# Kernel optimization log

Measured on AMD Instinct MI355X. Metric: run time of the kernel, lower is better.

Reference implementation:

```python
import jax, jax.numpy as jnp
import numpy as np
from jax import lax

EPS = 1e-5

def _conv(x, w, pad):
    return lax.conv_general_dilated(
        x, w, window_strides=(1, 1), padding=[(pad, pad), (pad, pad)],
        dimension_numbers=('NCHW', 'OIHW', 'NCHW'))

def _bn(x, p):
    # p: [4, C] rows = gamma, beta, running_mean, running_var (inference BN)
    g, b, m, v = p[0], p[1], p[2], p[3]
    scale = g / jnp.sqrt(v + EPS)
    return x * scale[None, :, None, None] + (b - m * scale)[None, :, None, None]

def _cbr(x, w, p, relu=True):
    y = _bn(_conv(x, w, pad=1), p)
    return jax.nn.relu(y) if relu else y

def _make_bn(key, c):
    k1, k2, k3 = jax.random.split(key, 3)
    gamma = jnp.ones((c,), jnp.float32) + 0.05 * jax.random.normal(k1, (c,))
    beta = 0.1 * jax.random.normal(k2, (c,))
    mean = 0.1 * jax.random.normal(k3, (c,))
    var = jax.random.uniform(k1, (c,), minval=0.5, maxval=1.5)
    return jnp.stack([gamma, beta, mean, var]).astype(jnp.float32)

def setup_inputs() -> dict:
    key = jax.random.key(0)
    ks = jax.random.split(key, 12)
    C, M = 256, 64  # channels, bottleneck width (hard-coded 64 in source)
    B, H, W = 8, 128, 128
    s = lambda fan: 1.0 / np.sqrt(fan)
    return {
        'x': jax.random.normal(ks[0], (B, C, H, W), jnp.float32),
        'w_res': jax.random.normal(ks[1], (C, C, 1, 1), jnp.float32) * s(C),
        'bn_res': _make_bn(ks[2], C),
        'w_vpre': jax.random.normal(ks[3], (M, C, 3, 3), jnp.float32) * s(C * 9),
        'bn_vpre': _make_bn(ks[4], M),
        'w_hpre': jax.random.normal(ks[5], (M, C, 3, 3), jnp.float32) * s(C * 9),
        'bn_hpre': _make_bn(ks[6], M),
        'w_add': jax.random.normal(ks[7], (C, M, 3, 3), jnp.float32) * s(M * 9),
        'bn_add': _make_bn(ks[8], C),
        'w_post': jax.random.normal(ks[9], (C, C, 3, 3), jnp.float32) * s(C * 9),
        'bn_post': _make_bn(ks[10], C),
    }

def reference(x, w_res, bn_res, w_vpre, bn_vpre, w_hpre, bn_hpre,
              w_add, bn_add, w_post, bn_post):
    # residual branch: 1x1 conv + BN (no relu)
    res = _bn(_conv(x, w_res, pad=0), bn_res)
    # vertical branch: conv-bn-relu then TopPool (reverse cumulative max over H)
    p1 = _cbr(x, w_vpre, bn_vpre)
    pool1 = lax.cummax(p1, axis=2, reverse=True)
    # horizontal branch: conv-bn-relu then LeftPool (reverse cumulative max over W)
    p2 = _cbr(x, w_hpre, bn_hpre)
    pool2 = lax.cummax(p2, axis=3, reverse=True)
    # merge: conv-bn (no relu), residual add, relu, post conv-bn-relu
    merged = _cbr(pool1 + pool2, w_add, bn_add, relu=False)
    out = jax.nn.relu(res + merged)
    return _cbr(out, w_post, bn_post)
```

## Files before the change

### kernel.cpp

```cpp
#include <hip/hip_runtime.h>
#include <hip/hip_bf16.h>


using bf16x8  = __attribute__((ext_vector_type(8))) __bf16;
using floatx4 = __attribute__((ext_vector_type(4))) float;

typedef __attribute__((address_space(1))) const uint32_t gas_u32;
typedef __attribute__((address_space(3))) uint32_t las_u32;

__device__ __forceinline__ float bf2f(__hip_bfloat16 h) { return __bfloat162float(h); }
__device__ __forceinline__ __hip_bfloat16 f2bf(float f) { return __float2bfloat16(f); }


__global__ __launch_bounds__(256) void k_cast_x(const float* __restrict__ x,
                                                __hip_bfloat16* __restrict__ xb) {
    __shared__ float t[64][65];
    const int n  = blockIdx.z;
    const int h  = blockIdx.y;
    const int c0 = (blockIdx.x >> 1) * 64;
    const int w0 = (blockIdx.x & 1) * 64;
    const int tid = threadIdx.x;
#pragma unroll
    for (int it = 0; it < 16; ++it) {
        int idx = it * 256 + tid;
        int c = idx >> 6, w = idx & 63;
        t[c][w] = x[(((size_t)n * 256 + c0 + c) * 128 + h) * 128 + w0 + w];
    }
    __syncthreads();
#pragma unroll
    for (int it = 0; it < 16; ++it) {
        int idx = it * 256 + tid;
        int w = idx >> 6, c = idx & 63;
        xb[(((size_t)n * 128 + h) * 128 + w0 + w) * 256 + c0 + c] = f2bf(t[c][w]);
    }
}

__global__ void k_prep_bn(const float* __restrict__ p, float* __restrict__ sc,
                          float* __restrict__ bi, int C) {
    int i = blockIdx.x * 64 + threadIdx.x;
    if (i >= C) return;
    float g = p[i], b = p[C + i], m = p[2 * C + i], v = p[3 * C + i];
    float s = g / sqrtf(v + 1e-5f);
    sc[i] = s;
    bi[i] = b - m * s;
}

__global__ void k_reorder_w3(const float* __restrict__ src, __hip_bfloat16* __restrict__ dst,
                             const float* __restrict__ scale, int Cin, int CoutTot,
                             int co_off, int total) {
    int i = blockIdx.x * 256 + threadIdx.x;
    if (i >= total) return;
    int ci  = i % Cin;
    int tap = (i / Cin) % 9;
    int co  = i / (Cin * 9);
    dst[((((size_t)tap * (Cin >> 5) + (ci >> 5)) * CoutTot) + co_off + co) * 32 + (ci & 31)] =
        f2bf(src[((size_t)co * Cin + ci) * 9 + tap] * scale[co]);
}

__global__ void k_reorder_w1(const float* __restrict__ src, __hip_bfloat16* __restrict__ dst,
                             const float* __restrict__ scale, int Cin, int total) {
    int i = blockIdx.x * 256 + threadIdx.x;
    if (i >= total) return;
    dst[i] = f2bf(src[i] * scale[i / Cin]);
}


__global__ __launch_bounds__(256) void k_pool1(__hip_bfloat16* __restrict__ b) {
    const int idx = blockIdx.x * 256 + threadIdx.x;
    const int c = idx & 63;
    const int w = (idx >> 6) & 127;
    const int n = idx >> 13;
    const size_t stride = 128 * 64;
    const size_t base = ((size_t)n * 128 * 128 + w) * 64 + c;
    float m = 0.0f;
    for (int hb = 31; hb >= 0; --hb) {
        size_t a0 = base + (size_t)(4 * hb) * stride;
        float v0 = bf2f(b[a0]);
        float v1 = bf2f(b[a0 + stride]);
        float v2 = bf2f(b[a0 + 2 * stride]);
        float v3 = bf2f(b[a0 + 3 * stride]);
        float m3 = fmaxf(m, v3);
        float m2 = fmaxf(m3, v2);
        float m1 = fmaxf(m2, v1);
        float m0 = fmaxf(m1, v0);
        b[a0 + 3 * stride] = f2bf(m3);
        b[a0 + 2 * stride] = f2bf(m2);
        b[a0 + stride]     = f2bf(m1);
        b[a0]              = f2bf(m0);
        m = m0;
    }
}

__global__ __launch_bounds__(256) void k_pool2(__hip_bfloat16* __restrict__ b,
                                               const __hip_bfloat16* __restrict__ pl) {
    const int idx = blockIdx.x * 256 + threadIdx.x;
    const int c = idx & 63;
    const int h = (idx >> 6) & 127;
    const int n = idx >> 13;
    const size_t base = (((size_t)n * 128 + h) * 128) * 64 + c;
    float m = 0.0f;
    for (int wb = 31; wb >= 0; --wb) {
        size_t a0 = base + (size_t)(4 * wb) * 64;
        float v0 = bf2f(b[a0]);
        float v1 = bf2f(b[a0 + 64]);
        float v2 = bf2f(b[a0 + 128]);
        float v3 = bf2f(b[a0 + 192]);
        float u0 = bf2f(pl[a0]);
        float u1 = bf2f(pl[a0 + 64]);
        float u2 = bf2f(pl[a0 + 128]);
        float u3 = bf2f(pl[a0 + 192]);
        float m3 = fmaxf(m, v3);
        float m2 = fmaxf(m3, v2);
        float m1 = fmaxf(m2, v1);
        float m0 = fmaxf(m1, v0);
        b[a0 + 192] = f2bf(m3 + u3);
        b[a0 + 128] = f2bf(m2 + u2);
        b[a0 + 64]  = f2bf(m1 + u1);
        b[a0]       = f2bf(m0 + u0);
        m = m0;
    }
}

__global__ __launch_bounds__(256) void conv1x1(const __hip_bfloat16* __restrict__ xin,
                                               const __hip_bfloat16* __restrict__ wgt,
                                               const float* __restrict__ bias,
                                               __hip_bfloat16* __restrict__ out) {
    __shared__ __align__(16) __hip_bfloat16 Xs[128 * 64];
    __shared__ __align__(16) __hip_bfloat16 Ws[128 * 64];
    const int tid  = threadIdx.x;
    const int lane = tid & 63;
    const int wid  = tid >> 6;
    const int wm = wid >> 1, wn = wid & 1;
    const int p0 = blockIdx.x * 128;
    const int c0 = blockIdx.y * 128;
    const int q = lane >> 4, r16 = lane & 15;

    floatx4 acc[4][4] = {};

    for (int k0 = 0; k0 < 256; k0 += 64) {
#pragma unroll
        for (int it = 0; it < 4; ++it) {
            const int pp = it * 32 + (tid >> 3);
            const int g  = tid & 7;
            uint4 val = *(const uint4*)(xin + ((size_t)(p0 + pp) * 256 + k0 + g * 8));
            *(uint4*)(&Xs[pp * 64 + (((g + pp) & 7) * 8)]) = val;
        }
#pragma unroll
        for (int it = 0; it < 4; ++it) {
            const int rr = it * 32 + (tid >> 3);
            const int g  = tid & 7;
            uint4 val = *(const uint4*)(wgt + ((size_t)(c0 + rr) * 256 + k0 + g * 8));
            *(uint4*)(&Ws[rr * 64 + (((g + rr) & 7) * 8)]) = val;
        }
        __syncthreads();
#pragma unroll
        for (int ks = 0; ks < 2; ++ks) {
            bf16x8 afr[4], bfr[4];
#pragma unroll
            for (int i = 0; i < 4; ++i) {
                const int pp = wm * 64 + i * 16 + r16;
                const int g  = ks * 4 + q;
                afr[i] = *(const bf16x8*)(&Xs[pp * 64 + (((g + pp) & 7) * 8)]);
            }
#pragma unroll
            for (int j = 0; j < 4; ++j) {
                const int rr = wn * 64 + j * 16 + r16;
                const int g  = ks * 4 + q;
                bfr[j] = *(const bf16x8*)(&Ws[rr * 64 + (((g + rr) & 7) * 8)]);
            }
#pragma unroll
            for (int i = 0; i < 4; ++i)
#pragma unroll
                for (int j = 0; j < 4; ++j)
                    acc[i][j] = __builtin_amdgcn_mfma_f32_16x16x32_bf16(afr[i], bfr[j], acc[i][j], 0, 0, 0);
        }
        __syncthreads();
    }
#pragma unroll
    for (int j = 0; j < 4; ++j) {
        const int co = c0 + wn * 64 + j * 16 + r16;
        const float bi = bias[co];
#pragma unroll
        for (int i = 0; i < 4; ++i) {
            const int pb = p0 + wm * 64 + i * 16 + q * 4;
#pragma unroll
            for (int r = 0; r < 4; ++r)
                out[(size_t)(pb + r) * 256 + co] = f2bf(acc[i][j][r] + bi);
        }
    }
}

template <int CIN, int COUT, int MODE>
__global__ __launch_bounds__(512, 2) void conv3x3(const __hip_bfloat16* __restrict__ xin,
                                                  const __hip_bfloat16* __restrict__ wgt,
                                                  const float* __restrict__ bias,
                                                  void* __restrict__ out,
                                                  const __hip_bfloat16* __restrict__ resbuf,
                                                  __hip_bfloat16* __restrict__ out2) {
    constexpr int NCH = CIN / 32;
    __shared__ __align__(16) __hip_bfloat16 Xs[6 * 130 * 32];
    __shared__ __align__(16) __hip_bfloat16 Ws[9 * 128 * 32];
    const int tid  = threadIdx.x;
    const int lane = tid & 63;
    const int wid  = tid >> 6;
    const int wm   = wid >> 1;
    const int wn   = wid & 1;
    const int bx   = blockIdx.x;
    const int n     = bx >> 5;
    const int hbase = (bx & 31) * 4;
    const int co_off = blockIdx.y * 128;
    const int q = lane >> 4, r16 = lane & 15;

    const int le = lane >> 2, lp = lane & 3;
    const int xe = wid * 16 + 1 + le;
    const int xg = (lp - ((xe >> 1) & 3)) & 3;
    const int xlaneoff = (xe - 1) * CIN + xg * 8;
    const int wrow = wid * 16 + le;
    const int wg2 = (lp - ((wrow >> 1) & 3)) & 3;
    const int wlaneoff = wrow * 32 + wg2 * 8;

    floatx4 acc[4][2][4] = {};

    auto stage = [&](int c) {
        const int ci0 = c * 32;
#pragma unroll
        for (int r = 0; r < 6; ++r) {
            const int hh = hbase - 1 + r;
            if (0 <= hh && hh < 128) {
                const __hip_bfloat16* src =
                    xin + ((size_t)(n * 128 + hh) * 128) * CIN + ci0 + xlaneoff;
                __builtin_amdgcn_global_load_lds((gas_u32*)src,
                    (las_u32*)&Xs[((size_t)r * 130 + wid * 16 + 1) * 32], 16, 0, 0);
            } else {
                *(uint4*)(&Xs[((size_t)r * 130 + xe) * 32 + lp * 8]) =
                    make_uint4(0u, 0u, 0u, 0u);
            }
        }
#pragma unroll
        for (int tap = 0; tap < 9; ++tap) {
            const __hip_bfloat16* src =
                wgt + ((size_t)(tap * NCH + c) * COUT + co_off) * 32 + wlaneoff;
            __builtin_amdgcn_global_load_lds((gas_u32*)src,
                (las_u32*)&Ws[((size_t)tap * 128 + wid * 16) * 32], 16, 0, 0);
        }
    };

    if (tid < 48) {
        int r = tid >> 3, side = (tid >> 2) & 1, p = tid & 3;
        *(uint4*)(&Xs[((size_t)r * 130 + (side ? 129 : 0)) * 32 + p * 8]) =
            make_uint4(0u, 0u, 0u, 0u);
    }
    stage(0);
    __syncthreads();

    for (int c = 0; c < NCH; ++c) {
#pragma unroll
        for (int tap = 0; tap < 9; ++tap) {
            const int tr = tap / 3, dw = tap % 3 - 1;
            bf16x8 bfr[4];
#pragma unroll
            for (int j = 0; j < 4; ++j) {
                const int row = wn * 64 + j * 16 + r16;
                const int pg  = (q + ((row >> 1) & 3)) & 3;
                bfr[j] = *(const bf16x8*)(&Ws[((size_t)tap * 128 + row) * 32 + pg * 8]);
            }
#pragma unroll
            for (int row = 0; row < 4; ++row) {
                bf16x8 afr[2];
#pragma unroll
                for (int i = 0; i < 2; ++i) {
                    const int e  = wm * 32 + i * 16 + r16 + dw + 1;
                    const int pg = (q + ((e >> 1) & 3)) & 3;
                    afr[i] = *(const bf16x8*)(&Xs[((size_t)(row + tr) * 130 + e) * 32 + pg * 8]);
                }
#pragma unroll
                for (int i = 0; i < 2; ++i)
#pragma unroll
                    for (int j = 0; j < 4; ++j) {
                        if (MODE == 3)
                            acc[row][i][j] = __builtin_amdgcn_mfma_f32_16x16x32_bf16(bfr[j], afr[i], acc[row][i][j], 0, 0, 0);
                        else
                            acc[row][i][j] = __builtin_amdgcn_mfma_f32_16x16x32_bf16(afr[i], bfr[j], acc[row][i][j], 0, 0, 0);
                    }
            }
        }
        __syncthreads();
        if (c + 1 < NCH) {
            stage(c + 1);
            __syncthreads();
        }
    }

    if (MODE == 1) {
#pragma unroll
        for (int row = 0; row < 4; ++row) {
            const int h = hbase + row;
#pragma unroll
            for (int j = 0; j < 4; ++j) {
                const int co = wn * 64 + j * 16 + r16;
                const float bi = bias[co];
                __hip_bfloat16* ob = (co < 64) ? (__hip_bfloat16*)out : out2;
                const int ch = co & 63;
#pragma unroll
                for (int i = 0; i < 2; ++i) {
#pragma unroll
                    for (int r = 0; r < 4; ++r) {
                        const int w = wm * 32 + i * 16 + q * 4 + r;
                        const size_t p = (size_t)(n * 128 + h) * 128 + w;
                        ob[p * 64 + ch] = f2bf(fmaxf(acc[row][i][j][r] + bi, 0.0f));
                    }
                }
            }
        }
    } else if (MODE == 2) {
        __hip_bfloat16* o = (__hip_bfloat16*)out;
#pragma unroll
        for (int row = 0; row < 4; ++row) {
            const int h = hbase + row;
#pragma unroll
            for (int j = 0; j < 4; ++j) {
                const int co = co_off + wn * 64 + j * 16 + r16;
                const float bi = bias[co];
#pragma unroll
                for (int i = 0; i < 2; ++i) {
#pragma unroll
                    for (int r = 0; r < 4; ++r) {
                        const int w = wm * 32 + i * 16 + q * 4 + r;
                        const size_t p = (size_t)(n * 128 + h) * 128 + w;
                        float v = acc[row][i][j][r] + bi + bf2f(resbuf[p * 256 + co]);
                        o[p * 256 + co] = f2bf(fmaxf(v, 0.0f));
                    }
                }
            }
        }
    } else {
        float* o = (float*)out;
#pragma unroll
        for (int row = 0; row < 4; ++row) {
            const int h = hbase + row;
#pragma unroll
            for (int j = 0; j < 4; ++j) {
#pragma unroll
                for (int r = 0; r < 4; ++r) {
                    const int co = co_off + wn * 64 + j * 16 + q * 4 + r;
                    const float bi = bias[co];
#pragma unroll
                    for (int i = 0; i < 2; ++i) {
                        const int w = wm * 32 + i * 16 + r16;
                        float v = fmaxf(acc[row][i][j][r] + bi, 0.0f);
                        o[(((size_t)(n * 256 + co)) * 128 + h) * 128 + w] = v;
                    }
                }
            }
        }
    }
}


extern "C" void kernel_launch(void* const* d_in, const int* in_sizes, int n_in,
                              void* d_out, int out_size, void* d_ws, size_t ws_size,
                              hipStream_t stream) {
    const float* x       = (const float*)d_in[0];
    const float* w_res   = (const float*)d_in[1];
    const float* bn_res  = (const float*)d_in[2];
    const float* w_vpre  = (const float*)d_in[3];
    const float* bn_vpre = (const float*)d_in[4];
    const float* w_hpre  = (const float*)d_in[5];
    const float* bn_hpre = (const float*)d_in[6];
    const float* w_add   = (const float*)d_in[7];
    const float* bn_add  = (const float*)d_in[8];
    const float* w_post  = (const float*)d_in[9];
    const float* bn_post = (const float*)d_in[10];

    const size_t SZ_XB = (size_t)8 * 128 * 128 * 256 * 2;
    const size_t SZ_P  = (size_t)8 * 128 * 128 * 64 * 2;

    char* w = (char*)d_ws;
    __hip_bfloat16* xb   = (__hip_bfloat16*)(w);
    __hip_bfloat16* resb = (__hip_bfloat16*)(w + SZ_XB);
    __hip_bfloat16* p1   = (__hip_bfloat16*)(w + 2 * SZ_XB);
    __hip_bfloat16* p2   = (__hip_bfloat16*)(w + 2 * SZ_XB + SZ_P);
    char* wp = w + 2 * SZ_XB + 2 * SZ_P;
    __hip_bfloat16* wres  = (__hip_bfloat16*)wp; wp += (size_t)65536 * 2;
    __hip_bfloat16* wpre  = (__hip_bfloat16*)wp; wp += (size_t)9 * 128 * 256 * 2;
    __hip_bfloat16* wadd  = (__hip_bfloat16*)wp; wp += (size_t)9 * 256 * 64 * 2;
    __hip_bfloat16* wpost = (__hip_bfloat16*)wp; wp += (size_t)9 * 256 * 256 * 2;
    float* sc_res  = (float*)wp; wp += 256 * 4;
    float* bi_res  = (float*)wp; wp += 256 * 4;
    float* sc_pre  = (float*)wp; wp += 128 * 4;
    float* bi_pre  = (float*)wp; wp += 128 * 4;
    float* sc_add  = (float*)wp; wp += 256 * 4;
    float* bi_add  = (float*)wp; wp += 256 * 4;
    float* sc_post = (float*)wp; wp += 256 * 4;
    float* bi_post = (float*)wp; wp += 256 * 4;

    k_prep_bn<<<4, 64, 0, stream>>>(bn_res, sc_res, bi_res, 256);
    k_prep_bn<<<1, 64, 0, stream>>>(bn_vpre, sc_pre, bi_pre, 64);
    k_prep_bn<<<1, 64, 0, stream>>>(bn_hpre, sc_pre + 64, bi_pre + 64, 64);
    k_prep_bn<<<4, 64, 0, stream>>>(bn_add, sc_add, bi_add, 256);
    k_prep_bn<<<4, 64, 0, stream>>>(bn_post, sc_post, bi_post, 256);

    k_reorder_w1<<<256, 256, 0, stream>>>(w_res, wres, sc_res, 256, 65536);
    k_reorder_w3<<<576, 256, 0, stream>>>(w_vpre, wpre, sc_pre, 256, 128, 0, 147456);
    k_reorder_w3<<<576, 256, 0, stream>>>(w_hpre, wpre, sc_pre + 64, 256, 128, 64, 147456);
    k_reorder_w3<<<576, 256, 0, stream>>>(w_add, wadd, sc_add, 64, 256, 0, 147456);
    k_reorder_w3<<<2304, 256, 0, stream>>>(w_post, wpost, sc_post, 256, 256, 0, 589824);

    k_cast_x<<<dim3(8, 128, 8), 256, 0, stream>>>(x, xb);

    conv1x1<<<dim3(1024, 2), 256, 0, stream>>>(xb, wres, bi_res, resb);
    conv3x3<256, 128, 1><<<dim3(256, 1), 512, 0, stream>>>(xb, wpre, bi_pre, p1, nullptr, p2);
    k_pool1<<<256, 256, 0, stream>>>(p1);
    k_pool2<<<256, 256, 0, stream>>>(p2, p1);
    conv3x3<64, 256, 2><<<dim3(256, 2), 512, 0, stream>>>(p2, wadd, bi_add, xb, resb, nullptr);
    conv3x3<256, 256, 3><<<dim3(256, 2), 512, 0, stream>>>(xb, wpost, bi_post, d_out, nullptr, nullptr);
}
```

Baseline: 412.0 us.

## Double-buffer conv3x3 LDS staging with per-tap-row weight phases and prefetch

Splits each input-channel chunk into three phases (one per kernel row) and double-buffers both the input tile and a three-tap weight slice in LDS. The loads for the next phase are issued before computing the current one, and only one barrier is used per phase. This aims to hide global-to-LDS load latency behind MFMA work instead of serializing load and compute. It adds LDS footprint and more frequent barriers.

```diff
diff --git a/kernel.cpp b/kernel.cpp
--- a/kernel.cpp
+++ b/kernel.cpp
@@ -198,8 +198,9 @@
                                                   const __hip_bfloat16* __restrict__ resbuf,
                                                   __hip_bfloat16* __restrict__ out2) {
     constexpr int NCH = CIN / 32;
-    __shared__ __align__(16) __hip_bfloat16 Xs[6 * 130 * 32];
-    __shared__ __align__(16) __hip_bfloat16 Ws[9 * 128 * 32];
+    constexpr int NPH = 3 * NCH;
+    __shared__ __align__(16) __hip_bfloat16 Xs[2][6 * 130 * 32];
+    __shared__ __align__(16) __hip_bfloat16 Ws[2][3 * 128 * 32];
     const int tid  = threadIdx.x;
     const int lane = tid & 63;
     const int wid  = tid >> 6;
@@ -221,8 +222,9 @@
 
     floatx4 acc[4][2][4] = {};
 
-    auto stage = [&](int c) {
+    auto stageX = [&](int c) {
         const int ci0 = c * 32;
+        __hip_bfloat16* xbuf = Xs[c & 1];
 #pragma unroll
         for (int r = 0; r < 6; ++r) {
             const int hh = hbase - 1 + r;
@@ -230,63 +232,75 @@
                 const __hip_bfloat16* src =
                     xin + ((size_t)(n * 128 + hh) * 128) * CIN + ci0 + xlaneoff;
                 __builtin_amdgcn_global_load_lds((gas_u32*)src,
-                    (las_u32*)&Xs[((size_t)r * 130 + wid * 16 + 1) * 32], 16, 0, 0);
+                    (las_u32*)&xbuf[((size_t)r * 130 + wid * 16 + 1) * 32], 16, 0, 0);
             } else {
-                *(uint4*)(&Xs[((size_t)r * 130 + xe) * 32 + lp * 8]) =
+                *(uint4*)(&xbuf[((size_t)r * 130 + xe) * 32 + lp * 8]) =
                     make_uint4(0u, 0u, 0u, 0u);
             }
         }
-#pragma unroll
-        for (int tap = 0; tap < 9; ++tap) {
+    };
+    auto stageW = [&](int ph) {
+        const int t0 = (ph % 3) * 3;
+        const int c  = ph / 3;
+        __hip_bfloat16* wbuf = Ws[ph & 1];
+#pragma unroll
+        for (int t = 0; t < 3; ++t) {
             const __hip_bfloat16* src =
-                wgt + ((size_t)(tap * NCH + c) * COUT + co_off) * 32 + wlaneoff;
+                wgt + ((size_t)((t0 + t) * NCH + c) * COUT + co_off) * 32 + wlaneoff;
             __builtin_amdgcn_global_load_lds((gas_u32*)src,
-                (las_u32*)&Ws[((size_t)tap * 128 + wid * 16) * 32], 16, 0, 0);
+                (las_u32*)&wbuf[((size_t)t * 128 + wid * 16) * 32], 16, 0, 0);
         }
     };
 
-    if (tid < 48) {
-        int r = tid >> 3, side = (tid >> 2) & 1, p = tid & 3;
-        *(uint4*)(&Xs[((size_t)r * 130 + (side ? 129 : 0)) * 32 + p * 8]) =
+    if (tid < 96) {
+        int b = tid / 48, rem = tid % 48;
+        int r = rem >> 3, side = (rem >> 2) & 1, p = rem & 3;
+        *(uint4*)(&Xs[b][((size_t)r * 130 + (side ? 129 : 0)) * 32 + p * 8]) =
             make_uint4(0u, 0u, 0u, 0u);
     }
-    stage(0);
+    stageX(0);
+    stageW(0);
     __syncthreads();
 
     for (int c = 0; c < NCH; ++c) {
 #pragma unroll
-        for (int tap = 0; tap < 9; ++tap) {
-            const int tr = tap / 3, dw = tap % 3 - 1;
-            bf16x8 bfr[4];
-#pragma unroll
-            for (int j = 0; j < 4; ++j) {
-                const int row = wn * 64 + j * 16 + r16;
-                const int pg  = (q + ((row >> 1) & 3)) & 3;
-                bfr[j] = *(const bf16x8*)(&Ws[((size_t)tap * 128 + row) * 32 + pg * 8]);
-            }
-#pragma unroll
-            for (int row = 0; row < 4; ++row) {
-                bf16x8 afr[2];
-#pragma unroll
-                for (int i = 0; i < 2; ++i) {
-                    const int e  = wm * 32 + i * 16 + r16 + dw + 1;
-                    const int pg = (q + ((e >> 1) & 3)) & 3;
-                    afr[i] = *(const bf16x8*)(&Xs[((size_t)(row + tr) * 130 + e) * 32 + pg * 8]);
+        for (int k = 0; k < 3; ++k) {
+            const int p = 3 * c + k;
+            if (p + 1 < NPH) stageW(p + 1);
+            if (k == 0 && c + 1 < NCH) stageX(c + 1);
+            __builtin_amdgcn_sched_barrier(0);
+            const __hip_bfloat16* xbuf = Xs[c & 1];
+            const __hip_bfloat16* wbuf = Ws[p & 1];
+#pragma unroll
+            for (int t = 0; t < 3; ++t) {
+                const int dw = t - 1;
+                bf16x8 bfr[4];
+#pragma unroll
+                for (int j = 0; j < 4; ++j) {
+                    const int row = wn * 64 + j * 16 + r16;
+                    const int pg  = (q + ((row >> 1) & 3)) & 3;
+                    bfr[j] = *(const bf16x8*)(&wbuf[((size_t)t * 128 + row) * 32 + pg * 8]);
                 }
 #pragma unroll
-                for (int i = 0; i < 2; ++i)
-#pragma unroll
-                    for (int j = 0; j < 4; ++j) {
-                        if (MODE == 3)
-                            acc[row][i][j] = __builtin_amdgcn_mfma_f32_16x16x32_bf16(bfr[j], afr[i], acc[row][i][j], 0, 0, 0);
-                        else
-                            acc[row][i][j] = __builtin_amdgcn_mfma_f32_16x16x32_bf16(afr[i], bfr[j], acc[row][i][j], 0, 0, 0);
+                for (int row = 0; row < 4; ++row) {
+                    bf16x8 afr[2];
+#pragma unroll
+                    for (int i = 0; i < 2; ++i) {
+                        const int e  = wm * 32 + i * 16 + r16 + dw + 1;
+                        const int pg = (q + ((e >> 1) & 3)) & 3;
+                        afr[i] = *(const bf16x8*)(&xbuf[((size_t)(row + k) * 130 + e) * 32 + pg * 8]);
                     }
-            }
-        }
-        __syncthreads();
-        if (c + 1 < NCH) {
-            stage(c + 1);
+#pragma unroll
+                    for (int i = 0; i < 2; ++i)
+#pragma unroll
+                        for (int j = 0; j < 4; ++j) {
+                            if (MODE == 3)
+                                acc[row][i][j] = __builtin_amdgcn_mfma_f32_16x16x32_bf16(bfr[j], afr[i], acc[row][i][j], 0, 0, 0);
+                            else
+                                acc[row][i][j] = __builtin_amdgcn_mfma_f32_16x16x32_bf16(afr[i], bfr[j], acc[row][i][j], 0, 0, 0);
+                        }
+                }
+            }
             __syncthreads();
         }
     }
```

Result: no change. 417.0 us (+1.2%).
